# Performance work log

Measured on AMD Instinct MI355X. Metric: run time of the kernel, lower is better.

The kernel has to match this reference:

```python
import math
import jax, jax.numpy as jnp
import numpy as np

ROUNDS = 4
BUCKET_LEN = 64
NEG_BIG = -1e9
NEG_SELF = -1e5
EPS = 1e-12


def look_back(x):
    # x: [B, n_buckets, bucket_len, ...]; prepend previous bucket (circular) along bucket_len axis
    return jnp.concatenate([jnp.roll(x, 1, axis=1), x], axis=2)


def gather_dim1(x, idx):
    # torch expand_gather: broadcast x and idx to common shape, gather along axis 1
    shape = np.broadcast_shapes(x.shape, idx.shape)
    return jnp.take_along_axis(jnp.broadcast_to(x, shape), jnp.broadcast_to(idx, shape), axis=1)


def setup_inputs() -> dict:
    key = jax.random.key(0)
    k1, k2, k3 = jax.random.split(key, 3)
    B, L, d_k = 16, 4096, 64
    n_buckets = L // BUCKET_LEN
    query = jax.random.normal(k1, (B, L, d_k), dtype=jnp.float32)
    value = jax.random.normal(k2, (B, L, d_k), dtype=jnp.float32)
    rand_matrix = jax.random.normal(k3, (B, d_k, ROUNDS, n_buckets // 2), dtype=jnp.float32)
    return {"query": query, "value": value, "rand_matrix": rand_matrix, "seed": 0}


def lsh_hashes(query, rand_matrix):
    # LocalitySensitiveHash.forward
    B, L, d_k = query.shape
    qn = query / jnp.maximum(jnp.linalg.norm(query, axis=-1, keepdims=True), EPS)
    rm = rand_matrix / jnp.linalg.norm(rand_matrix, axis=1, keepdims=True)
    mm = jnp.einsum('bld,bdrn->blrn', qn, rm)  # [B, L, rounds, n_buckets//2]
    h = jnp.argmax(jnp.concatenate([mm, -mm], axis=-1), axis=-1).astype(jnp.int32)  # [B, L, rounds]
    return h * L + jnp.arange(L, dtype=jnp.int32)[None, :, None]  # unique per position


def _lsh_attention(query, value, rand_matrix):
    B, L, d_k = query.shape
    R, bl = ROUNDS, BUCKET_LEN
    nb = L // bl

    h = lsh_hashes(query, rand_matrix)
    sorted_hashes = jnp.sort(h, axis=1)
    hash_indice = jnp.argsort(h, axis=1)               # [B, L, R]
    original_indice = jnp.argsort(hash_indice, axis=1)  # reverse_sort

    # reorder queries by hash, bucketize: [B, nb, bl, d_k, R]
    rq = gather_dim1(query[:, :, :, None], hash_indice[:, :, None, :]).reshape(B, nb, bl, d_k, R)
    lb_key = look_back(rq)
    lb_key = lb_key / jnp.maximum(jnp.linalg.norm(lb_key, axis=-2, keepdims=True), EPS)
    scores = jnp.einsum('bnidr,bnjdr->bnijr', rq, lb_key) / math.sqrt(d_k)  # [B, nb, bl, 2bl, R]

    # mask: different buckets, causal, self
    sh = sorted_hashes.reshape(B, nb, bl, R) // L  # bucket id
    scores = jnp.where(sh[..., None, :] != look_back(sh)[..., None, :, :], NEG_BIG, scores)
    qi = hash_indice.reshape(B, nb, bl, R).astype(jnp.int32)
    ki = look_back(qi)  # [B, nb, 2bl, R]
    scores = jnp.where(qi[..., None, :] < ki[..., None, :, :], NEG_BIG, scores)
    scores = jnp.where(qi[..., None, :] == ki[..., None, :, :], NEG_SELF, scores)

    # duplicate-key counting across rounds (get_dup_keys)
    ki_full = jnp.broadcast_to(ki[:, :, None, :, :], (B, nb, bl, 2 * bl, R)).reshape(B, L, 2 * bl, R)
    ki_full = gather_dim1(ki_full, original_indice[:, :, None, :])
    flat = ki_full.reshape(B, L, 2 * bl * R)
    s_idx = jnp.argsort(flat, axis=-1)
    s = jnp.take_along_axis(flat, s_idx, axis=-1)
    counts = jnp.ones_like(s)
    for i in range(1, R):
        eq = (s[..., i:] == s[..., :-i]).astype(s.dtype)
        counts = counts + jnp.pad(eq, ((0, 0), (0, 0), (i, 0))) + jnp.pad(eq, ((0, 0), (0, 0), (0, i)))
    inv = jnp.argsort(s_idx, axis=-1)
    count_key = jnp.take_along_axis(counts, inv, axis=-1).reshape(B, L, 2 * bl, R)
    count_key = gather_dim1(count_key, hash_indice[:, :, None, :])

    # duplicate-adjusted softmax
    scores = scores.reshape(B, L, 2 * bl, R)
    lse = jax.nn.logsumexp(scores, axis=2)  # [B, L, R]
    softmax_qk = jnp.exp(scores - jnp.log(count_key.astype(scores.dtype)) - lse[:, :, None, :])

    rv = gather_dim1(value[:, :, :, None], hash_indice[:, :, None, :]).reshape(B, nb, bl, d_k, R)
    sm = softmax_qk.reshape(B, nb, bl, 2 * bl, R)
    attn = jnp.einsum('bnijr,bnjdr->bnidr', sm, look_back(rv)).reshape(B, L, d_k, R)
    attn = gather_dim1(attn, original_indice[:, :, None, :])
    lse = jnp.take_along_axis(lse, original_indice, axis=1)
    round_weights = jax.nn.softmax(lse, axis=1)  # dim=1 (length) exactly as in the source
    return jnp.einsum('bldr,blr->bld', attn, round_weights)


def reference(query, value, rand_matrix, seed):
    # seed is unused by the original forward body; dropout skipped (eval mode)
    return _lsh_attention(query, value, rand_matrix)
```

## Files before the change

kernel.cpp:

```cpp
#include <hip/hip_runtime.h>
#include <math.h>

#define B_  16
#define L_  4096
#define D_  64
#define R_  4
#define NB_ 64
#define BL_ 64
#define FIXCAP 8192

typedef _Float16 f16x8 __attribute__((ext_vector_type(8)));
typedef _Float16 f16x2 __attribute__((ext_vector_type(2)));
typedef float    f32x4 __attribute__((ext_vector_type(4)));


__global__ __launch_bounds__(64) void k_rmnorm(const float* __restrict__ rm,
                                               double* __restrict__ rmn,
                                               _Float16* __restrict__ rhi_g,
                                               _Float16* __restrict__ rlo_g,
                                               int* __restrict__ fix_cnt) {
    if (blockIdx.x == 0 && threadIdx.x == 0) *fix_cnt = 0;
    int blk = blockIdx.x;
    int b = blk >> 7, r = (blk >> 5) & 3, n = blk & 31;
    int d = threadIdx.x;
    double v = (double)rm[(((size_t)b * 64 + d) * 4 + r) * 32 + n];
    double sq = v * v;
    #pragma unroll
    for (int off = 32; off > 0; off >>= 1) sq += __shfl_down(sq, off);
    double tot = __shfl(sq, 0);
    double nv = v / sqrt(tot);
    rmn[(((size_t)b * 4 + r) * 32 + n) * 64 + d] = nv;
    float f = (float)nv;
    _Float16 hi = (_Float16)f;
    size_t gi = ((size_t)b * 128 + r * 32 + n) * 64 + d;
    rhi_g[gi] = hi;
    rlo_g[gi] = (_Float16)(f - (float)hi);
}

__global__ __launch_bounds__(256, 4) void k_hash(const float* __restrict__ q,
                                                 const _Float16* __restrict__ rhi_g,
                                                 const _Float16* __restrict__ rlo_g,
                                                 int* __restrict__ h_ws,
                                                 int* __restrict__ fix_cnt,
                                                 int* __restrict__ fix_list) {
    __shared__ __align__(16) char smem[36864];
    _Float16* Rhi = (_Float16*)smem;
    _Float16* Rlo = (_Float16*)(smem + 18432);
    float*    Sc  = (float*)smem;

    int blk = blockIdx.x;
    int b = blk >> 6, chunk = blk & 63;
    int tid = threadIdx.x;
    int w = tid >> 6, lane = tid & 63, quad = lane >> 4, l15 = lane & 15;

    {
        int row = tid >> 1, dh = (tid & 1) * 32;
        const _Float16* sh = rhi_g + ((size_t)b * 128 + row) * 64 + dh;
        const _Float16* sl = rlo_g + ((size_t)b * 128 + row) * 64 + dh;
        #pragma unroll
        for (int g = 0; g < 4; g++) {
            *(f16x8*)&Rhi[row * 72 + dh + g * 8] = *(const f16x8*)(sh + g * 8);
            *(f16x8*)&Rlo[row * 72 + dh + g * 8] = *(const f16x8*)(sl + g * 8);
        }
    }

    int qrow = chunk * 64 + w * 16 + l15;
    const float* qp = q + ((size_t)(b * L_ + qrow)) * 64;
    f16x8 Ahi[2], Alo[2];
    #pragma unroll
    for (int kt = 0; kt < 2; kt++) {
        float4 t0 = *(const float4*)(qp + kt * 32 + quad * 8);
        float4 t1 = *(const float4*)(qp + kt * 32 + quad * 8 + 4);
        float fv[8] = {t0.x, t0.y, t0.z, t0.w, t1.x, t1.y, t1.z, t1.w};
        #pragma unroll
        for (int j = 0; j < 8; j++) {
            _Float16 hi = (_Float16)fv[j];
            Ahi[kt][j] = hi;
            Alo[kt][j] = (_Float16)(fv[j] - (float)hi);
        }
    }
    __syncthreads();

    f32x4 acc[8];
    #pragma unroll
    for (int jt = 0; jt < 8; jt++) acc[jt] = (f32x4){0.f, 0.f, 0.f, 0.f};
    #pragma unroll
    for (int jt = 0; jt < 8; jt++) {
        #pragma unroll
        for (int kt = 0; kt < 2; kt++) {
            f16x8 bh = *(const f16x8*)&Rhi[(jt * 16 + l15) * 72 + kt * 32 + quad * 8];
            f16x8 bl = *(const f16x8*)&Rlo[(jt * 16 + l15) * 72 + kt * 32 + quad * 8];
            acc[jt] = __builtin_amdgcn_mfma_f32_16x16x32_f16(Ahi[kt], bh, acc[jt], 0, 0, 0);
            acc[jt] = __builtin_amdgcn_mfma_f32_16x16x32_f16(Ahi[kt], bl, acc[jt], 0, 0, 0);
            acc[jt] = __builtin_amdgcn_mfma_f32_16x16x32_f16(Alo[kt], bh, acc[jt], 0, 0, 0);
        }
    }
    __syncthreads();

    #pragma unroll
    for (int jt = 0; jt < 8; jt++) {
        #pragma unroll
        for (int reg = 0; reg < 4; reg++)
            Sc[(w * 16 + quad * 4 + reg) * 133 + jt * 16 + l15] = acc[jt][reg];
    }
    __syncthreads();

    {
        int row = tid & 63, r = tid >> 6;
        const float* sp = &Sc[row * 133 + r * 32];
        float bp = -1e30f, bn = -1e30f; int ip = 0, in2 = 0;
        float v1 = -1e30f, v2 = -1e30f;
        #pragma unroll
        for (int n = 0; n < 32; n++) {
            float v = sp[n], nv = -v;
            if (v > bp)  { bp = v;  ip = n; }
            if (nv > bn) { bn = nv; in2 = n; }
            if (v > v1)       { v2 = v1; v1 = v; }
            else if (v > v2)  { v2 = v; }
            if (nv > v1)      { v2 = v1; v1 = nv; }
            else if (nv > v2) { v2 = nv; }
        }
        int i1 = (bp >= bn) ? ip : (32 + in2);
        int l = chunk * 64 + row;
        h_ws[((size_t)(b * 4 + r)) * L_ + l] = i1;
        if (v1 - v2 < 4e-5f) {
            int slot = atomicAdd(fix_cnt, 1);
            if (slot < FIXCAP) fix_list[slot] = (b << 14) | (r << 12) | l;
        }
    }
}

__global__ __launch_bounds__(64) void k_fix(const float* __restrict__ q,
                                            const double* __restrict__ rmn,
                                            const int* __restrict__ fix_cnt,
                                            const int* __restrict__ fix_list,
                                            int* __restrict__ h_ws) {
    int cnt = *fix_cnt; if (cnt > FIXCAP) cnt = FIXCAP;
    int lane = threadIdx.x;
    for (int i = blockIdx.x; i < cnt; i += gridDim.x) {
        int e = fix_list[i];
        int b = e >> 14, r = (e >> 12) & 3, l = e & 4095;
        int n = lane & 31;
        const double* rp = rmn + ((size_t)(b * 4 + r)) * 2048 + n * 64;
        const float* qr = q + ((size_t)(b * L_ + l)) * 64;
        double a0 = 0.0, a1 = 0.0, a2 = 0.0, a3 = 0.0;
        #pragma unroll
        for (int d = 0; d < 64; d += 4) {
            a0 += (double)qr[d]   * rp[d];
            a1 += (double)qr[d+1] * rp[d+1];
            a2 += (double)qr[d+2] * rp[d+2];
            a3 += (double)qr[d+3] * rp[d+3];
        }
        double acc = ((a0 + a1) + (a2 + a3));
        double v = (lane < 32) ? acc : -acc;
        int idx = lane;
        #pragma unroll
        for (int off = 1; off < 64; off <<= 1) {
            double ov = __shfl_xor(v, off);
            int   oidx = __shfl_xor(idx, off);
            if (ov > v || (ov == v && oidx < idx)) { v = ov; idx = oidx; }
        }
        if (lane == 0) h_ws[((size_t)(b * 4 + r)) * L_ + l] = idx;
    }
}

__global__ __launch_bounds__(64) void k_sort(const int* __restrict__ h_ws,
                                             int* __restrict__ hi_ws,
                                             int* __restrict__ oi_ws) {
    __shared__ int hs[64 * 65];
    __shared__ int cnt[64 * 65];
    int br = blockIdx.x;
    const int* hp = h_ws + (size_t)br * L_;
    int t = threadIdx.x;
    for (int w = 0; w < 64; w++) hs[w * 65 + t] = hp[w * 64 + t];
    for (int u = 0; u < 64; u++) cnt[t * 65 + u] = 0;
    __syncthreads();
    for (int k = 0; k < 64; k++) cnt[t * 65 + hs[t * 65 + k]]++;
    __syncthreads();
    int cs = 0;
    for (int c = 0; c < 64; c++) cs += cnt[c * 65 + t];
    int v = cs;
    #pragma unroll
    for (int off = 1; off < 64; off <<= 1) {
        int u = __shfl_up(v, off);
        if (t >= off) v += u;
    }
    int running = v - cs;
    for (int c = 0; c < 64; c++) {
        int tmp = cnt[c * 65 + t];
        cnt[c * 65 + t] = running;
        running += tmp;
    }
    __syncthreads();
    int* hi = hi_ws + (size_t)br * L_;
    int* oi = oi_ws + (size_t)br * L_;
    for (int k = 0; k < 64; k++) {
        int idx = t * 64 + k;
        int b2 = hs[t * 65 + k];
        int pos = cnt[t * 65 + b2]++;
        hi[pos] = idx;
        oi[idx] = pos;
    }
}

__global__ __launch_bounds__(256) void k_meta(const int* __restrict__ h_ws,
                                              const int* __restrict__ hi_ws,
                                              const int* __restrict__ oi_ws,
                                              int4* __restrict__ meta_ws) {
    int gid = blockIdx.x * 256 + threadIdx.x;
    int br = gid >> 12, spos = gid & 4095;
    int b = br >> 2;
    int p = hi_ws[(size_t)br * L_ + spos];
    int hh = h_ws[(size_t)br * L_ + p];
    int pack = 0, packm1 = 0;
    #pragma unroll
    for (int r2 = 0; r2 < 4; r2++) {
        int bk = oi_ws[((size_t)(b * 4 + r2)) * L_ + p] >> 6;
        pack   |= bk << (8 * r2);
        packm1 |= ((bk + 63) & 63) << (8 * r2);
    }
    meta_ws[(size_t)br * L_ + spos] = make_int4(hh, p, pack, packm1);
}

__global__ __launch_bounds__(256, 4) void k_attn(const float* __restrict__ query,
                                                 const float* __restrict__ value,
                                                 const int4* __restrict__ meta_ws,
                                                 float* __restrict__ lse_ws,
                                                 _Float16* __restrict__ attn_ws) {
    __shared__ _Float16 Ksh[128 * 72];
    __shared__ _Float16 Vt[64 * 136];
    __shared__ int4 kmeta[128];

    int xcd = blockIdx.x & 7, slot = blockIdx.x >> 3;
    int b = xcd * 2 + (slot >> 8);
    int rem = slot & 255, n = rem >> 2, r = rem & 3;
    int tid = threadIdx.x;
    int w = tid >> 6, lane = tid & 63, quad = lane >> 4, l15 = lane & 15;
    int hibase = (b * 4 + r) * L_;

    if (tid < 128) {
        int j = tid;
        int nprev = (n + 63) & 63;
        int spos = (j < 64) ? (nprev * 64 + j) : (n * 64 + (j - 64));
        kmeta[j] = meta_ws[hibase + spos];
    }
    __syncthreads();

    {
        int j = tid >> 1, dh = (tid & 1) * 32;
        int p = kmeta[j].y;
        const float4* qrow = (const float4*)(query + ((size_t)(b * L_ + p)) * 64 + dh);
        float qv[32];
        float ss = 0.f;
        #pragma unroll
        for (int c = 0; c < 8; c++) {
            float4 t = qrow[c];
            qv[4*c+0] = t.x; qv[4*c+1] = t.y; qv[4*c+2] = t.z; qv[4*c+3] = t.w;
            ss += t.x*t.x + t.y*t.y + t.z*t.z + t.w*t.w;
        }
        ss += __shfl_xor(ss, 1);
        float nr = sqrtf(ss); if (nr < 1e-12f) nr = 1e-12f;
        float kscale = 0.125f / nr;
        #pragma unroll
        for (int g = 0; g < 4; g++) {
            f16x8 hv;
            #pragma unroll
            for (int t2 = 0; t2 < 8; t2++) hv[t2] = (_Float16)(qv[g*8+t2] * kscale);
            *(f16x8*)&Ksh[j * 72 + dh + g * 8] = hv;
        }
    }
    {
        int m = tid >> 2, sub = tid & 3;
        int p0 = kmeta[2 * m].y, p1 = kmeta[2 * m + 1].y;
        const float4* v0p = (const float4*)(value + ((size_t)(b * L_ + p0)) * 64 + sub * 16);
        const float4* v1p = (const float4*)(value + ((size_t)(b * L_ + p1)) * 64 + sub * 16);
        float a0[16], a1[16];
        #pragma unroll
        for (int c = 0; c < 4; c++) {
            float4 t0 = v0p[c], t1 = v1p[c];
            a0[4*c+0]=t0.x; a0[4*c+1]=t0.y; a0[4*c+2]=t0.z; a0[4*c+3]=t0.w;
            a1[4*c+0]=t1.x; a1[4*c+1]=t1.y; a1[4*c+2]=t1.z; a1[4*c+3]=t1.w;
        }
        #pragma unroll
        for (int d = 0; d < 16; d++) {
            f16x2 hv = { (_Float16)a0[d], (_Float16)a1[d] };
            *(f16x2*)&Vt[(sub * 16 + d) * 136 + 2 * m] = hv;
        }
    }

    int4 qmw = kmeta[64 + w * 16 + l15];
    const float* qp = query + ((size_t)(b * L_ + qmw.y)) * 64;
    f16x8 afr[2];
    #pragma unroll
    for (int kt = 0; kt < 2; kt++) {
        float4 t0 = *(const float4*)(qp + kt * 32 + quad * 8);
        float4 t1 = *(const float4*)(qp + kt * 32 + quad * 8 + 4);
        float fv[8] = {t0.x, t0.y, t0.z, t0.w, t1.x, t1.y, t1.z, t1.w};
        #pragma unroll
        for (int j = 0; j < 8; j++) afr[kt][j] = (_Float16)fv[j];
    }
    __syncthreads();

    f32x4 acc[8];
    #pragma unroll
    for (int jt = 0; jt < 8; jt++) acc[jt] = (f32x4){0.f, 0.f, 0.f, 0.f};
    #pragma unroll
    for (int jt = 0; jt < 8; jt++) {
        #pragma unroll
        for (int kt = 0; kt < 2; kt++) {
            f16x8 bfr = *(const f16x8*)&Ksh[(jt * 16 + l15) * 72 + kt * 32 + quad * 8];
            acc[jt] = __builtin_amdgcn_mfma_f32_16x16x32_f16(afr[kt], bfr, acc[jt], 0, 0, 0);
        }
    }

    int4 qm4[4], km4[8];
    #pragma unroll
    for (int reg = 0; reg < 4; reg++) qm4[reg] = kmeta[64 + w * 16 + quad * 4 + reg];
    #pragma unroll
    for (int jt = 0; jt < 8; jt++) km4[jt] = kmeta[jt * 16 + l15];
    __syncthreads();

    _Float16* Ph = Ksh;
    float lse_r[4];
    #pragma unroll
    for (int reg = 0; reg < 4; reg++) {
        float s[8];
        #pragma unroll
        for (int jt = 0; jt < 8; jt++) {
            float v = acc[jt][reg];
            if (km4[jt].x != qm4[reg].x) v = -1e9f;
            if (qm4[reg].y < km4[jt].y)  v = -1e9f;
            if (qm4[reg].y == km4[jt].y) v = -1e5f;
            s[jt] = v;
        }
        float m = s[0];
        #pragma unroll
        for (int jt = 1; jt < 8; jt++) m = fmaxf(m, s[jt]);
        #pragma unroll
        for (int off = 1; off < 16; off <<= 1) m = fmaxf(m, __shfl_xor(m, off));
        float te[8], sum = 0.f;
        #pragma unroll
        for (int jt = 0; jt < 8; jt++) { te[jt] = __expf(s[jt] - m); sum += te[jt]; }
        #pragma unroll
        for (int off = 1; off < 16; off <<= 1) sum += __shfl_xor(sum, off);
        float inv = 1.f / sum;
        lse_r[reg] = m + __logf(sum);
        int i = w * 16 + quad * 4 + reg;
        #pragma unroll
        for (int jt = 0; jt < 8; jt++) {
            int z1 = km4[jt].z ^ qm4[reg].z;
            int z2 = km4[jt].z ^ qm4[reg].w;
            int nz = __popc((z1 + 0x7f7f7f7f) & 0x80808080)
                   + __popc((z2 + 0x7f7f7f7f) & 0x80808080);
            float p = te[jt] * inv / (float)(8 - nz);
            Ph[i * 136 + jt * 16 + l15] = (_Float16)p;
        }
    }
    if (l15 == 0) {
        #pragma unroll
        for (int reg = 0; reg < 4; reg++)
            lse_ws[hibase + qm4[reg].y] = lse_r[reg];
    }
    __syncthreads();

    f32x4 oacc[4];
    #pragma unroll
    for (int nt = 0; nt < 4; nt++) oacc[nt] = (f32x4){0.f, 0.f, 0.f, 0.f};
    #pragma unroll
    for (int kt = 0; kt < 4; kt++) {
        f16x8 pa = *(const f16x8*)&Ph[(w * 16 + l15) * 136 + kt * 32 + quad * 8];
        #pragma unroll
        for (int nt = 0; nt < 4; nt++) {
            f16x8 vb = *(const f16x8*)&Vt[(nt * 16 + l15) * 136 + kt * 32 + quad * 8];
            oacc[nt] = __builtin_amdgcn_mfma_f32_16x16x32_f16(pa, vb, oacc[nt], 0, 0, 0);
        }
    }
    #pragma unroll
    for (int reg = 0; reg < 4; reg++) {
        size_t base = (((size_t)(b * 4 + r)) * L_ + qm4[reg].y) * 64;
        #pragma unroll
        for (int nt = 0; nt < 4; nt++)
            attn_ws[base + nt * 16 + l15] = (_Float16)oacc[nt][reg];
    }
}

__global__ __launch_bounds__(256) void k_rw(const float* __restrict__ lse_ws,
                                            float* __restrict__ rwmax,
                                            float* __restrict__ rwsum) {
    __shared__ float  red[256];
    __shared__ double redd[256];
    int br = blockIdx.x;
    const float* lp = lse_ws + (size_t)br * L_;
    int t = threadIdx.x;
    float m = -1e30f;
    for (int k = t; k < L_; k += 256) m = fmaxf(m, lp[k]);
    red[t] = m; __syncthreads();
    for (int s2 = 128; s2 > 0; s2 >>= 1) {
        if (t < s2) red[t] = fmaxf(red[t], red[t + s2]);
        __syncthreads();
    }
    float mm = red[0];
    double s = 0.0;
    for (int k = t; k < L_; k += 256) s += (double)expf(lp[k] - mm);
    redd[t] = s; __syncthreads();
    for (int s2 = 128; s2 > 0; s2 >>= 1) {
        if (t < s2) redd[t] += redd[t + s2];
        __syncthreads();
    }
    if (t == 0) { rwmax[br] = mm; rwsum[br] = (float)redd[0]; }
}

__global__ __launch_bounds__(256) void k_out(const _Float16* __restrict__ attn_ws,
                                             const float* __restrict__ lse_ws,
                                             const float* __restrict__ rwmax,
                                             const float* __restrict__ rwsum,
                                             float* __restrict__ out) {
    int gid = blockIdx.x * 256 + threadIdx.x;
    int g = gid & 7;
    size_t row = (size_t)(gid >> 3);
    int b = (int)(row >> 12), l = (int)(row & 4095);
    float o[8];
    #pragma unroll
    for (int k = 0; k < 8; k++) o[k] = 0.f;
    #pragma unroll
    for (int r = 0; r < 4; r++) {
        int br = b * 4 + r;
        float wgt = __expf(lse_ws[(size_t)br * L_ + l] - rwmax[br]) / rwsum[br];
        f16x8 av = *(const f16x8*)&attn_ws[(((size_t)br * L_ + l) << 6) + g * 8];
        #pragma unroll
        for (int k = 0; k < 8; k++) o[k] += (float)av[k] * wgt;
    }
    float4* op = (float4*)(out + row * 64 + g * 8);
    op[0] = make_float4(o[0], o[1], o[2], o[3]);
    op[1] = make_float4(o[4], o[5], o[6], o[7]);
}

extern "C" void kernel_launch(void* const* d_in, const int* in_sizes, int n_in,
                              void* d_out, int out_size, void* d_ws, size_t ws_size,
                              hipStream_t stream) {
    const float* query = (const float*)d_in[0];
    const float* value = (const float*)d_in[1];
    const float* rm    = (const float*)d_in[2];
    char* ws = (char*)d_ws;
    double*    rmn    = (double*)ws;
    int*       h_ws   = (int*)(ws + ((size_t)1 << 20));
    int*       hi_ws  = (int*)(ws + ((size_t)2 << 20));
    int*       oi_ws  = (int*)(ws + ((size_t)3 << 20));
    float*     lse_ws = (float*)(ws + ((size_t)4 << 20));
    float*     rwmax  = (float*)(ws + ((size_t)5 << 20));
    float*     rwsum  = (float*)(ws + ((size_t)5 << 20) + 256);
    int*       fix_cnt= (int*)(ws + ((size_t)5 << 20) + 512);
    int*       fix_list=(int*)(ws + ((size_t)5 << 20) + 1024);
    _Float16*  attn_ws= (_Float16*)(ws + ((size_t)6 << 20));
    _Float16*  rhi_g  = (_Float16*)(ws + ((size_t)40 << 20));
    _Float16*  rlo_g  = (_Float16*)(ws + ((size_t)41 << 20));
    int4*      meta_ws= (int4*)(ws + ((size_t)44 << 20));
    float*     out    = (float*)d_out;

    hipLaunchKernelGGL(k_rmnorm, dim3(2048), dim3(64),  0, stream, rm, rmn, rhi_g, rlo_g, fix_cnt);
    hipLaunchKernelGGL(k_hash,   dim3(1024), dim3(256), 0, stream, query, rhi_g, rlo_g,
                       h_ws, fix_cnt, fix_list);
    hipLaunchKernelGGL(k_fix,    dim3(64),   dim3(64),  0, stream, query, rmn,
                       fix_cnt, fix_list, h_ws);
    hipLaunchKernelGGL(k_sort,   dim3(64),   dim3(64),  0, stream, h_ws, hi_ws, oi_ws);
    hipLaunchKernelGGL(k_meta,   dim3(1024), dim3(256), 0, stream, h_ws, hi_ws, oi_ws, meta_ws);
    hipLaunchKernelGGL(k_attn,   dim3(4096), dim3(256), 0, stream,
                       query, value, meta_ws, lse_ws, attn_ws);
    hipLaunchKernelGGL(k_rw,     dim3(64),   dim3(256), 0, stream, lse_ws, rwmax, rwsum);
    hipLaunchKernelGGL(k_out,    dim3(2048), dim3(256), 0, stream,
                       attn_ws, lse_ws, rwmax, rwsum, out);
}
```

Before: 175.9 us.

## Precompute fp16 query, normalized key and value in hash kernel for attention

The hash kernel now also writes fp16 copies of the query, the L2-normalized and scaled key, and the value into workspace. The attention kernel gathers these half-precision rows instead of reloading fp32 rows and normalizing/converting them per block, which happens 4 rounds × 2 (look-back) times per row. This halves the gather bytes in attention and removes redundant norm/convert work, at the cost of extra writes in the hash kernel. Divisions are also replaced with hardware reciprocal approximations in the softmax and output weighting.

```diff
diff --git a/kernel.cpp b/kernel.cpp
--- a/kernel.cpp
+++ b/kernel.cpp
@@ -38,11 +38,15 @@
 }
 
 __global__ __launch_bounds__(256, 4) void k_hash(const float* __restrict__ q,
+                                                 const float* __restrict__ value,
                                                  const _Float16* __restrict__ rhi_g,
                                                  const _Float16* __restrict__ rlo_g,
                                                  int* __restrict__ h_ws,
                                                  int* __restrict__ fix_cnt,
-                                                 int* __restrict__ fix_list) {
+                                                 int* __restrict__ fix_list,
+                                                 _Float16* __restrict__ qhf,
+                                                 _Float16* __restrict__ khf,
+                                                 _Float16* __restrict__ vhf) {
     __shared__ __align__(16) char smem[36864];
     _Float16* Rhi = (_Float16*)smem;
     _Float16* Rlo = (_Float16*)(smem + 18432);
@@ -54,6 +58,22 @@
     int w = tid >> 6, lane = tid & 63, quad = lane >> 4, l15 = lane & 15;
 
     {
+        int row = chunk * 64 + (tid >> 2), sub = tid & 3;
+        const float4* vp = (const float4*)(value + ((size_t)(b * L_ + row)) * 64 + sub * 16);
+        f16x8 h0, h1;
+        #pragma unroll
+        for (int c = 0; c < 2; c++) {
+            float4 t0 = vp[2 * c], t1 = vp[2 * c + 1];
+            f16x8& hd = c ? h1 : h0;
+            hd[0]=(_Float16)t0.x; hd[1]=(_Float16)t0.y; hd[2]=(_Float16)t0.z; hd[3]=(_Float16)t0.w;
+            hd[4]=(_Float16)t1.x; hd[5]=(_Float16)t1.y; hd[6]=(_Float16)t1.z; hd[7]=(_Float16)t1.w;
+        }
+        _Float16* dst = vhf + ((size_t)(b * L_ + row)) * 64 + sub * 16;
+        *(f16x8*)dst = h0;
+        *(f16x8*)(dst + 8) = h1;
+    }
+
+    {
         int row = tid >> 1, dh = (tid & 1) * 32;
         const _Float16* sh = rhi_g + ((size_t)b * 128 + row) * 64 + dh;
         const _Float16* sl = rlo_g + ((size_t)b * 128 + row) * 64 + dh;
@@ -66,17 +86,41 @@
 
     int qrow = chunk * 64 + w * 16 + l15;
     const float* qp = q + ((size_t)(b * L_ + qrow)) * 64;
-    f16x8 Ahi[2], Alo[2];
+    float qv[16];
     #pragma unroll
     for (int kt = 0; kt < 2; kt++) {
         float4 t0 = *(const float4*)(qp + kt * 32 + quad * 8);
         float4 t1 = *(const float4*)(qp + kt * 32 + quad * 8 + 4);
-        float fv[8] = {t0.x, t0.y, t0.z, t0.w, t1.x, t1.y, t1.z, t1.w};
+        qv[8*kt+0]=t0.x; qv[8*kt+1]=t0.y; qv[8*kt+2]=t0.z; qv[8*kt+3]=t0.w;
+        qv[8*kt+4]=t1.x; qv[8*kt+5]=t1.y; qv[8*kt+6]=t1.z; qv[8*kt+7]=t1.w;
+    }
+    f16x8 Ahi[2], Alo[2];
+    #pragma unroll
+    for (int kt = 0; kt < 2; kt++) {
         #pragma unroll
         for (int j = 0; j < 8; j++) {
-            _Float16 hi = (_Float16)fv[j];
+            _Float16 hi = (_Float16)qv[8*kt+j];
             Ahi[kt][j] = hi;
-            Alo[kt][j] = (_Float16)(fv[j] - (float)hi);
+            Alo[kt][j] = (_Float16)(qv[8*kt+j] - (float)hi);
+        }
+    }
+    {
+        float ss = 0.f;
+        #pragma unroll
+        for (int j = 0; j < 16; j++) ss += qv[j] * qv[j];
+        ss += __shfl_xor(ss, 16);
+        ss += __shfl_xor(ss, 32);
+        float nr = sqrtf(ss); if (nr < 1e-12f) nr = 1e-12f;
+        float kscale = 0.125f / nr;
+        _Float16* qd = qhf + ((size_t)(b * L_ + qrow)) * 64;
+        _Float16* kd = khf + ((size_t)(b * L_ + qrow)) * 64;
+        #pragma unroll
+        for (int kt = 0; kt < 2; kt++) {
+            *(f16x8*)(qd + kt * 32 + quad * 8) = Ahi[kt];
+            f16x8 hv;
+            #pragma unroll
+            for (int j = 0; j < 8; j++) hv[j] = (_Float16)(qv[8*kt+j] * kscale);
+            *(f16x8*)(kd + kt * 32 + quad * 8) = hv;
         }
     }
     __syncthreads();
@@ -222,8 +266,9 @@
     meta_ws[(size_t)br * L_ + spos] = make_int4(hh, p, pack, packm1);
 }
 
-__global__ __launch_bounds__(256, 4) void k_attn(const float* __restrict__ query,
-                                                 const float* __restrict__ value,
+__global__ __launch_bounds__(256, 4) void k_attn(const _Float16* __restrict__ qhf,
+                                                 const _Float16* __restrict__ khf,
+                                                 const _Float16* __restrict__ vhf,
                                                  const int4* __restrict__ meta_ws,
                                                  float* __restrict__ lse_ws,
                                                  _Float16* __restrict__ attn_ws) {
@@ -248,57 +293,31 @@
 
     {
         int j = tid >> 1, dh = (tid & 1) * 32;
-        int p = kmeta[j].y;
-        const float4* qrow = (const float4*)(query + ((size_t)(b * L_ + p)) * 64 + dh);
-        float qv[32];
-        float ss = 0.f;
-        #pragma unroll
-        for (int c = 0; c < 8; c++) {
-            float4 t = qrow[c];
-            qv[4*c+0] = t.x; qv[4*c+1] = t.y; qv[4*c+2] = t.z; qv[4*c+3] = t.w;
-            ss += t.x*t.x + t.y*t.y + t.z*t.z + t.w*t.w;
-        }
-        ss += __shfl_xor(ss, 1);
-        float nr = sqrtf(ss); if (nr < 1e-12f) nr = 1e-12f;
-        float kscale = 0.125f / nr;
-        #pragma unroll
-        for (int g = 0; g < 4; g++) {
-            f16x8 hv;
-            #pragma unroll
-            for (int t2 = 0; t2 < 8; t2++) hv[t2] = (_Float16)(qv[g*8+t2] * kscale);
-            *(f16x8*)&Ksh[j * 72 + dh + g * 8] = hv;
-        }
+        const _Float16* src = khf + ((size_t)(b * L_ + kmeta[j].y)) * 64 + dh;
+        #pragma unroll
+        for (int g = 0; g < 4; g++)
+            *(f16x8*)&Ksh[j * 72 + dh + g * 8] = *(const f16x8*)(src + g * 8);
     }
     {
         int m = tid >> 2, sub = tid & 3;
-        int p0 = kmeta[2 * m].y, p1 = kmeta[2 * m + 1].y;
-        const float4* v0p = (const float4*)(value + ((size_t)(b * L_ + p0)) * 64 + sub * 16);
-        const float4* v1p = (const float4*)(value + ((size_t)(b * L_ + p1)) * 64 + sub * 16);
-        float a0[16], a1[16];
-        #pragma unroll
-        for (int c = 0; c < 4; c++) {
-            float4 t0 = v0p[c], t1 = v1p[c];
-            a0[4*c+0]=t0.x; a0[4*c+1]=t0.y; a0[4*c+2]=t0.z; a0[4*c+3]=t0.w;
-            a1[4*c+0]=t1.x; a1[4*c+1]=t1.y; a1[4*c+2]=t1.z; a1[4*c+3]=t1.w;
-        }
-        #pragma unroll
-        for (int d = 0; d < 16; d++) {
-            f16x2 hv = { (_Float16)a0[d], (_Float16)a1[d] };
+        const _Float16* v0 = vhf + ((size_t)(b * L_ + kmeta[2 * m].y)) * 64 + sub * 16;
+        const _Float16* v1 = vhf + ((size_t)(b * L_ + kmeta[2 * m + 1].y)) * 64 + sub * 16;
+        f16x8 a00 = *(const f16x8*)v0, a01 = *(const f16x8*)(v0 + 8);
+        f16x8 a10 = *(const f16x8*)v1, a11 = *(const f16x8*)(v1 + 8);
+        #pragma unroll
+        for (int d = 0; d < 8; d++) {
+            f16x2 hv = { a00[d], a10[d] };
             *(f16x2*)&Vt[(sub * 16 + d) * 136 + 2 * m] = hv;
+            f16x2 hw = { a01[d], a11[d] };
+            *(f16x2*)&Vt[(sub * 16 + 8 + d) * 136 + 2 * m] = hw;
         }
     }
 
     int4 qmw = kmeta[64 + w * 16 + l15];
-    const float* qp = query + ((size_t)(b * L_ + qmw.y)) * 64;
+    const _Float16* qp = qhf + ((size_t)(b * L_ + qmw.y)) * 64;
     f16x8 afr[2];
-    #pragma unroll
-    for (int kt = 0; kt < 2; kt++) {
-        float4 t0 = *(const float4*)(qp + kt * 32 + quad * 8);
-        float4 t1 = *(const float4*)(qp + kt * 32 + quad * 8 + 4);
-        float fv[8] = {t0.x, t0.y, t0.z, t0.w, t1.x, t1.y, t1.z, t1.w};
-        #pragma unroll
-        for (int j = 0; j < 8; j++) afr[kt][j] = (_Float16)fv[j];
-    }
+    afr[0] = *(const f16x8*)(qp + quad * 8);
+    afr[1] = *(const f16x8*)(qp + 32 + quad * 8);
     __syncthreads();
 
     f32x4 acc[8];
@@ -343,7 +362,7 @@
         for (int jt = 0; jt < 8; jt++) { te[jt] = __expf(s[jt] - m); sum += te[jt]; }
         #pragma unroll
         for (int off = 1; off < 16; off <<= 1) sum += __shfl_xor(sum, off);
-        float inv = 1.f / sum;
+        float inv = __builtin_amdgcn_rcpf(sum);
         lse_r[reg] = m + __logf(sum);
         int i = w * 16 + quad * 4 + reg;
         #pragma unroll
@@ -352,7 +371,7 @@
             int z2 = km4[jt].z ^ qm4[reg].w;
             int nz = __popc((z1 + 0x7f7f7f7f) & 0x80808080)
                    + __popc((z2 + 0x7f7f7f7f) & 0x80808080);
-            float p = te[jt] * inv / (float)(8 - nz);
+            float p = te[jt] * inv * __builtin_amdgcn_rcpf((float)(8 - nz));
             Ph[i * 136 + jt * 16 + l15] = (_Float16)p;
         }
     }
@@ -425,7 +444,8 @@
     #pragma unroll
     for (int r = 0; r < 4; r++) {
         int br = b * 4 + r;
-        float wgt = __expf(lse_ws[(size_t)br * L_ + l] - rwmax[br]) / rwsum[br];
+        float wgt = __expf(lse_ws[(size_t)br * L_ + l] - rwmax[br])
+                  * __builtin_amdgcn_rcpf(rwsum[br]);
         f16x8 av = *(const f16x8*)&attn_ws[(((size_t)br * L_ + l) << 6) + g * 8];
         #pragma unroll
         for (int k = 0; k < 8; k++) o[k] += (float)av[k] * wgt;
@@ -453,19 +473,22 @@
     int*       fix_list=(int*)(ws + ((size_t)5 << 20) + 1024);
     _Float16*  attn_ws= (_Float16*)(ws + ((size_t)6 << 20));
     _Float16*  rhi_g  = (_Float16*)(ws + ((size_t)40 << 20));
-    _Float16*  rlo_g  = (_Float16*)(ws + ((size_t)41 << 20));
-    int4*      meta_ws= (int4*)(ws + ((size_t)44 << 20));
+    _Float16*  rlo_g  = (_Float16*)(ws + ((size_t)40 << 20) + ((size_t)1 << 19));
+    int4*      meta_ws= (int4*)(ws + ((size_t)41 << 20));
+    _Float16*  qhf    = (_Float16*)(ws + ((size_t)45 << 20));
+    _Float16*  khf    = (_Float16*)(ws + ((size_t)53 << 20));
+    _Float16*  vhf    = (_Float16*)(ws + ((size_t)61 << 20));
     float*     out    = (float*)d_out;
 
     hipLaunchKernelGGL(k_rmnorm, dim3(2048), dim3(64),  0, stream, rm, rmn, rhi_g, rlo_g, fix_cnt);
-    hipLaunchKernelGGL(k_hash,   dim3(1024), dim3(256), 0, stream, query, rhi_g, rlo_g,
-                       h_ws, fix_cnt, fix_list);
+    hipLaunchKernelGGL(k_hash,   dim3(1024), dim3(256), 0, stream, query, value, rhi_g, rlo_g,
+                       h_ws, fix_cnt, fix_list, qhf, khf, vhf);
     hipLaunchKernelGGL(k_fix,    dim3(64),   dim3(64),  0, stream, query, rmn,
                        fix_cnt, fix_list, h_ws);
     hipLaunchKernelGGL(k_sort,   dim3(64),   dim3(64),  0, stream, h_ws, hi_ws, oi_ws);
     hipLaunchKernelGGL(k_meta,   dim3(1024), dim3(256), 0, stream, h_ws, hi_ws, oi_ws, meta_ws);
     hipLaunchKernelGGL(k_attn,   dim3(4096), dim3(256), 0, stream,
-                       query, value, meta_ws, lse_ws, attn_ws);
+                       qhf, khf, vhf, meta_ws, lse_ws, attn_ws);
     hipLaunchKernelGGL(k_rw,     dim3(64),   dim3(256), 0, stream, lse_ws, rwmax, rwsum);
     hipLaunchKernelGGL(k_out,    dim3(2048), dim3(256), 0, stream,
                        attn_ws, lse_ws, rwmax, rwsum, out);
```

After: 167.6 us. 1.05x faster.
